# Kernel tuning notes

Measured on AMD Instinct MI355X. Metric: run time of the kernel, lower is better.

## Reference

```python
import jax, jax.numpy as jnp
import numpy as np

N = 50000   # total nodes
E = 600000  # total edges
F = 128     # in_features == hidden_features
H = 128
L = 4       # layers_count
B = 256     # number of graphs in batch
M = 200     # molecule_features
OUT = 12    # out_features
MH = H // 4 # molecular head width


def setup_inputs() -> dict:
    key = jax.random.key(0)
    ks = jax.random.split(key, 16)
    x = jax.random.normal(ks[0], (N, F), dtype=jnp.float32)
    edge_index = jax.random.randint(ks[1], (2, E), 0, N, dtype=jnp.int64)
    # sorted segment ids; guarantee every graph has >=1 node
    batch = jnp.sort(jnp.concatenate([
        jnp.arange(B, dtype=jnp.int64),
        jax.random.randint(ks[2], (N - B,), 0, B, dtype=jnp.int64)]))
    molecule_features = jax.random.normal(ks[3], (B, M), dtype=jnp.float32)
    s = 0.05
    Ws = jax.random.normal(ks[4], (L, H, H), dtype=jnp.float32) * s
    bs = jnp.zeros((L, H), dtype=jnp.float32)
    Wm = jax.random.normal(ks[5], (M, MH), dtype=jnp.float32) * s
    bm = jnp.zeros((MH,), dtype=jnp.float32)
    gamma = jnp.ones((MH,), dtype=jnp.float32)   # BatchNorm1d affine (eval mode, running stats 0/1)
    beta = jnp.zeros((MH,), dtype=jnp.float32)
    W1 = jax.random.normal(ks[6], (2 * H + MH, H), dtype=jnp.float32) * s  # mlp in = 288
    b1 = jnp.zeros((H,), dtype=jnp.float32)
    W2 = jax.random.normal(ks[7], (H, OUT), dtype=jnp.float32) * s
    b2 = jnp.zeros((OUT,), dtype=jnp.float32)
    return dict(x=x, edge_index=edge_index, batch=batch,
                molecule_features=molecule_features, Ws=Ws, bs=bs,
                Wm=Wm, bm=bm, gamma=gamma, beta=beta,
                W1=W1, b1=b1, W2=W2, b2=b2)


def gcn_conv(x, src, dst, W, b):
    # GCNConv: D^{-1/2} (A + I) D^{-1/2} X W + b, degrees include self loops
    ones = jnp.ones((E,), dtype=x.dtype)
    deg = jax.ops.segment_sum(ones, dst, num_segments=N) + 1.0  # self loop
    dis = jax.lax.rsqrt(deg)
    norm = dis[src] * dis[dst]                      # [E]
    xw = x @ W                                      # [N,H]
    msg = xw[src] * norm[:, None]                   # gather + scale
    agg = jax.ops.segment_sum(msg, dst, num_segments=N)
    agg = agg + xw * (dis * dis)[:, None]           # self-loop term
    return agg + b


def reference(x, edge_index, batch, molecule_features, Ws, bs, Wm, bm,
              gamma, beta, W1, b1, W2, b2):
    src, dst = edge_index[0], edge_index[1]
    h = x
    for l in range(L):
        y = jax.nn.relu(gcn_conv(h, src, dst, Ws[l], bs[l]))
        h = y + h  # residual (in == hidden); dropout is identity in eval
    max_pool = jax.ops.segment_max(h, batch, num_segments=B)
    add_pool = jax.ops.segment_sum(h, batch, num_segments=B)
    # molecular head: Linear -> Dropout(eval=identity) -> BatchNorm1d(eval) -> ReLU
    mol = molecule_features @ Wm + bm
    mol = jax.nn.relu(mol * gamma + beta)  # running_mean=0, running_var=1
    z = jnp.concatenate((max_pool, add_pool, mol), axis=1)  # [B, 288]
    z = jax.nn.relu(z @ W1 + b1)
    return z @ W2 + b2  # [B, OUT]
```

## Files before the change

kernel.cpp:

```cpp
#include <hip/hip_runtime.h>
#include <math.h>

static constexpr int NN  = 50000;
static constexpr int NE  = 600000;
static constexpr int HD  = 128;
static constexpr int NL  = 4;
static constexpr int NB  = 256;
static constexpr int NM  = 200;
static constexpr int NO  = 12;
static constexpr int NMH = 32;

#define MAX4(ac, b) { (ac).x = fmaxf((ac).x,(b).x); (ac).y = fmaxf((ac).y,(b).y); (ac).z = fmaxf((ac).z,(b).z); (ac).w = fmaxf((ac).w,(b).w); }
#define ADD4(ac, b) { (ac).x += (b).x; (ac).y += (b).y; (ac).z += (b).z; (ac).w += (b).w; }

typedef short bfx8 __attribute__((ext_vector_type(8)));
typedef float f32x4 __attribute__((ext_vector_type(4)));

__device__ __forceinline__ unsigned short f2bf(float f) {
  unsigned int u = __float_as_uint(f);
  unsigned int r = (u + 0x7fffu + ((u >> 16) & 1u)) >> 16;
  return (unsigned short)r;
}
__device__ __forceinline__ float bflo(unsigned int p) { return __uint_as_float(p << 16); }
__device__ __forceinline__ float bfhi(unsigned int p) { return __uint_as_float(p & 0xffff0000u); }

__global__ void k_hist(const int* __restrict__ dst, int* __restrict__ counts) {
  int e = blockIdx.x * blockDim.x + threadIdx.x;
  if (e < NE) atomicAdd(&counts[dst[e]], 1);
}

__global__ void k_dis(const int* __restrict__ counts, float* __restrict__ dis) {
  int i = blockIdx.x * blockDim.x + threadIdx.x;
  if (i < NN) dis[i] = rsqrtf((float)(counts[i] + 1));
}

__global__ void k_scan1(const int* __restrict__ counts, int* __restrict__ incl, int* __restrict__ bsum) {
  __shared__ int s[256];
  int i = blockIdx.x * 256 + threadIdx.x;
  int v = (i < NN) ? counts[i] : 0;
  s[threadIdx.x] = v;
  __syncthreads();
  for (int off = 1; off < 256; off <<= 1) {
    int t = (threadIdx.x >= off) ? s[threadIdx.x - off] : 0;
    __syncthreads();
    s[threadIdx.x] += t;
    __syncthreads();
  }
  if (i < NN) incl[i] = s[threadIdx.x];
  if (threadIdx.x == 255) bsum[blockIdx.x] = s[255];
}

__global__ void k_scan2(const int* __restrict__ bsum, int* __restrict__ boff, int nblocks) {
  __shared__ int s[256];
  int v = (threadIdx.x < nblocks) ? bsum[threadIdx.x] : 0;
  s[threadIdx.x] = v;
  __syncthreads();
  for (int off = 1; off < 256; off <<= 1) {
    int t = (threadIdx.x >= off) ? s[threadIdx.x - off] : 0;
    __syncthreads();
    s[threadIdx.x] += t;
    __syncthreads();
  }
  boff[threadIdx.x] = s[threadIdx.x] - v;
}

__global__ void k_scan3(const int* __restrict__ counts, int* __restrict__ rowst, const int* __restrict__ boff) {
  int i = blockIdx.x * 256 + threadIdx.x;
  if (i < NN) {
    rowst[i] = rowst[i] - counts[i] + boff[blockIdx.x];
    if (i == NN - 1) rowst[NN] = NE;
  }
}

__global__ void k_fill(const int* __restrict__ src, const int* __restrict__ dst,
                       const int* __restrict__ rowst, int* __restrict__ cur, int* __restrict__ csr) {
  int e = blockIdx.x * blockDim.x + threadIdx.x;
  if (e < NE) {
    int d = dst[e];
    int p = atomicAdd(&cur[d], 1);
    csr[rowst[d] + p] = src[e];
  }
}

__global__ void k_goffs(const int* __restrict__ batch, int* __restrict__ goffs) {
  int i = blockIdx.x * blockDim.x + threadIdx.x;
  if (i >= NN) return;
  int b = batch[i];
  if (i == 0) {
    for (int g = 0; g <= b; ++g) goffs[g] = 0;
  } else {
    int pb = batch[i - 1];
    for (int g = pb + 1; g <= b; ++g) goffs[g] = i;
  }
  if (i == NN - 1) goffs[NB] = NN;
}

__global__ void k_tobf(const float4* __restrict__ in, ushort4* __restrict__ outb, int n4) {
  int i = blockIdx.x * blockDim.x + threadIdx.x;
  if (i < n4) {
    float4 v = in[i];
    outb[i] = make_ushort4(f2bf(v.x), f2bf(v.y), f2bf(v.z), f2bf(v.w));
  }
}

__global__ void k_wT(const float* __restrict__ Ws, unsigned short* __restrict__ wT) {
  int i = blockIdx.x * blockDim.x + threadIdx.x;
  if (i < NL * HD * HD) {
    int l = i >> 14, rem = i & 16383, n = rem >> 7, k = rem & 127;
    wT[i] = f2bf(Ws[l * 16384 + k * 128 + n]);
  }
}

__launch_bounds__(256)
__global__ void k_gemm_mfma(const unsigned short* __restrict__ A,
                            const unsigned short* __restrict__ WT,
                            unsigned short* __restrict__ C) {
  const int wave = threadIdx.x >> 6;
  const int lane = threadIdx.x & 63;
  const int m_base = blockIdx.x * 128 + wave * 32;
  const int lr = lane & 15;
  const int kg = lane >> 4;

  f32x4 acc[2][8];
#pragma unroll
  for (int mi = 0; mi < 2; ++mi)
#pragma unroll
    for (int nj = 0; nj < 8; ++nj) acc[mi][nj] = (f32x4){0.f, 0.f, 0.f, 0.f};

  int ra0 = m_base + lr;       if (ra0 > NN - 1) ra0 = NN - 1;
  int ra1 = m_base + 16 + lr;  if (ra1 > NN - 1) ra1 = NN - 1;

#pragma unroll
  for (int kb = 0; kb < 4; ++kb) {
    const int k0 = kb * 32 + kg * 8;
    bfx8 a0 = *(const bfx8*)&A[(size_t)ra0 * HD + k0];
    bfx8 a1 = *(const bfx8*)&A[(size_t)ra1 * HD + k0];
#pragma unroll
    for (int nj = 0; nj < 8; ++nj) {
      bfx8 b = *(const bfx8*)&WT[(nj * 16 + lr) * HD + k0];
      acc[0][nj] = __builtin_amdgcn_mfma_f32_16x16x32_bf16(a0, b, acc[0][nj], 0, 0, 0);
      acc[1][nj] = __builtin_amdgcn_mfma_f32_16x16x32_bf16(a1, b, acc[1][nj], 0, 0, 0);
    }
  }

  const int col = lane & 15;
  const int rbase = (lane >> 4) * 4;
#pragma unroll
  for (int mi = 0; mi < 2; ++mi) {
#pragma unroll
    for (int r = 0; r < 4; ++r) {
      int row = m_base + mi * 16 + rbase + r;
      if (row < NN) {
#pragma unroll
        for (int nj = 0; nj < 8; ++nj) {
          C[(size_t)row * HD + nj * 16 + col] = f2bf(acc[mi][nj][r]);
        }
      }
    }
  }
}

__global__ void k_agg(const unsigned short* __restrict__ xw, const float* __restrict__ dis,
                      const int* __restrict__ rowst, const int* __restrict__ csr,
                      const float* __restrict__ bias, const float* __restrict__ hin,
                      float* __restrict__ hout, unsigned short* __restrict__ houtb) {
  int g = threadIdx.x >> 5;
  int lane = threadIdx.x & 31;
  int n = blockIdx.x * 8 + g;
  if (n >= NN) return;

  const uint2* xwb = (const uint2*)xw;

  float dn = dis[n];
  float4 acc;
  {
    uint2 p = xwb[(size_t)n * 32 + lane];
    float sl = dn * dn;
    acc.x = bflo(p.x) * sl; acc.y = bfhi(p.x) * sl;
    acc.z = bflo(p.y) * sl; acc.w = bfhi(p.y) * sl;
  }

  int s0 = rowst[n], s1 = rowst[n + 1];
  int idx = s0;
  for (; idx + 2 <= s1; idx += 2) {
    int sA = csr[idx], sB = csr[idx + 1];
    float nA = dis[sA] * dn;
    float nB = dis[sB] * dn;
    uint2 pA = xwb[(size_t)sA * 32 + lane];
    uint2 pB = xwb[(size_t)sB * 32 + lane];
    acc.x += nA * bflo(pA.x); acc.y += nA * bfhi(pA.x);
    acc.z += nA * bflo(pA.y); acc.w += nA * bfhi(pA.y);
    acc.x += nB * bflo(pB.x); acc.y += nB * bfhi(pB.x);
    acc.z += nB * bflo(pB.y); acc.w += nB * bfhi(pB.y);
  }
  if (idx < s1) {
    int sA = csr[idx];
    float nA = dis[sA] * dn;
    uint2 pA = xwb[(size_t)sA * 32 + lane];
    acc.x += nA * bflo(pA.x); acc.y += nA * bfhi(pA.x);
    acc.z += nA * bflo(pA.y); acc.w += nA * bfhi(pA.y);
  }

  float4 b4 = *(const float4*)&bias[lane * 4];
  float4 hv = *(const float4*)&hin[(size_t)n * HD + lane * 4];
  float4 out;
  out.x = fmaxf(acc.x + b4.x, 0.f) + hv.x;
  out.y = fmaxf(acc.y + b4.y, 0.f) + hv.y;
  out.z = fmaxf(acc.z + b4.z, 0.f) + hv.z;
  out.w = fmaxf(acc.w + b4.w, 0.f) + hv.w;
  *(float4*)&hout[(size_t)n * HD + lane * 4] = out;
  *(ushort4*)&houtb[(size_t)n * HD + lane * 4] =
      make_ushort4(f2bf(out.x), f2bf(out.y), f2bf(out.z), f2bf(out.w));
}

__launch_bounds__(1024)
__global__ void k_pool(const float* __restrict__ h, const int* __restrict__ goffs,
                       float* __restrict__ pooled) {
  __shared__ float4 smax[32][32];
  __shared__ float4 ssum[32][32];
  int g = blockIdx.x;
  int slot = threadIdx.x >> 5;
  int lane = threadIdx.x & 31;
  int a = goffs[g], bnd = goffs[g + 1];

  float4 mx = make_float4(-INFINITY, -INFINITY, -INFINITY, -INFINITY);
  float4 sm = make_float4(0.f, 0.f, 0.f, 0.f);
  for (int i = a + slot; i < bnd; i += 32) {
    float4 v = *(const float4*)&h[(size_t)i * HD + lane * 4];
    MAX4(mx, v);
    ADD4(sm, v);
  }
  smax[slot][lane] = mx;
  ssum[slot][lane] = sm;
  __syncthreads();
#pragma unroll
  for (int off = 16; off >= 1; off >>= 1) {
    if (slot < off) {
      float4 m2 = smax[slot + off][lane];
      float4 s2 = ssum[slot + off][lane];
      float4 m1 = smax[slot][lane];
      float4 s1 = ssum[slot][lane];
      MAX4(m1, m2);
      ADD4(s1, s2);
      smax[slot][lane] = m1;
      ssum[slot][lane] = s1;
    }
    __syncthreads();
  }
  if (slot == 0) {
    *(float4*)&pooled[g * 256 + lane * 4]       = smax[0][lane];
    *(float4*)&pooled[g * 256 + 128 + lane * 4] = ssum[0][lane];
  }
}

__global__ void k_head(const float* __restrict__ pooled, const float* __restrict__ mf,
                       const float* __restrict__ Wm, const float* __restrict__ bm,
                       const float* __restrict__ gamma, const float* __restrict__ beta,
                       const float* __restrict__ W1, const float* __restrict__ b1,
                       const float* __restrict__ W2, const float* __restrict__ b2,
                       float* __restrict__ out) {
  __shared__ float z[288];
  __shared__ float z1[128];
  int g = blockIdx.x, t = threadIdx.x;
  z[t] = pooled[g * 256 + t];
  z[128 + t] = pooled[g * 256 + 128 + t];
  if (t < NMH) {
    float acc = bm[t];
    for (int k = 0; k < NM; ++k) acc += mf[g * NM + k] * Wm[k * NMH + t];
    acc = acc * gamma[t] + beta[t];
    z[256 + t] = fmaxf(acc, 0.f);
  }
  __syncthreads();
  float acc = b1[t];
  for (int k = 0; k < 288; ++k) acc += z[k] * W1[k * HD + t];
  z1[t] = fmaxf(acc, 0.f);
  __syncthreads();
  if (t < NO) {
    float a2 = b2[t];
    for (int k = 0; k < HD; ++k) a2 += z1[k] * W2[k * NO + t];
    out[g * NO + t] = a2;
  }
}

extern "C" void kernel_launch(void* const* d_in, const int* in_sizes, int n_in,
                              void* d_out, int out_size, void* d_ws, size_t ws_size,
                              hipStream_t stream) {
  const float* x     = (const float*)d_in[0];
  const int*   eidx  = (const int*)d_in[1];
  const int*   batch = (const int*)d_in[2];
  const float* mf    = (const float*)d_in[3];
  const float* Ws    = (const float*)d_in[4];
  const float* bs    = (const float*)d_in[5];
  const float* Wm    = (const float*)d_in[6];
  const float* bm    = (const float*)d_in[7];
  const float* gamma = (const float*)d_in[8];
  const float* beta  = (const float*)d_in[9];
  const float* W1    = (const float*)d_in[10];
  const float* b1    = (const float*)d_in[11];
  const float* W2    = (const float*)d_in[12];
  const float* b2    = (const float*)d_in[13];
  float* out = (float*)d_out;

  const int* src = eidx;
  const int* dst = eidx + NE;

  char* w = (char*)d_ws;
  size_t off = 0;
  auto alloc = [&](size_t bytes) -> void* {
    void* p = w + off;
    off += (bytes + 255) & ~(size_t)255;
    return p;
  };
  float* dis    = (float*)alloc((size_t)NN * 4);
  float* h      = (float*)alloc((size_t)NN * HD * 4);
  unsigned short* xw  = (unsigned short*)alloc((size_t)NN * HD * 2);
  unsigned short* xbf = (unsigned short*)alloc((size_t)NN * HD * 2);
  unsigned short* hbf = (unsigned short*)alloc((size_t)NN * HD * 2);
  unsigned short* wT  = (unsigned short*)alloc((size_t)NL * HD * HD * 2);
  int* counts   = (int*)alloc((size_t)NN * 4);
  int* cur      = (int*)alloc((size_t)NN * 4);
  int* rowst    = (int*)alloc((size_t)(NN + 1) * 4);
  int* csr      = (int*)alloc((size_t)NE * 4);
  int* bsum     = (int*)alloc(256 * 4);
  int* boff     = (int*)alloc(256 * 4);
  int* goffs    = (int*)alloc((size_t)(NB + 1) * 4);
  float* pooled = (float*)alloc((size_t)NB * 256 * 4);
  (void)ws_size;

  const int SB = (NN + 255) / 256;

  hipMemsetAsync(counts, 0, (size_t)NN * 4, stream);
  hipMemsetAsync(cur, 0, (size_t)NN * 4, stream);

  k_hist<<<(NE + 255) / 256, 256, 0, stream>>>(dst, counts);
  k_dis<<<SB, 256, 0, stream>>>(counts, dis);
  k_scan1<<<SB, 256, 0, stream>>>(counts, rowst, bsum);
  k_scan2<<<1, 256, 0, stream>>>(bsum, boff, SB);
  k_scan3<<<SB, 256, 0, stream>>>(counts, rowst, boff);
  k_fill<<<(NE + 255) / 256, 256, 0, stream>>>(src, dst, rowst, cur, csr);

  k_goffs<<<SB, 256, 0, stream>>>(batch, goffs);
  k_tobf<<<((NN * HD / 4) + 255) / 256, 256, 0, stream>>>((const float4*)x, (ushort4*)xbf, NN * HD / 4);
  k_wT<<<(NL * HD * HD + 255) / 256, 256, 0, stream>>>(Ws, wT);

  for (int l = 0; l < NL; ++l) {
    const unsigned short* gin_bf = (l == 0) ? xbf : hbf;
    const float* resid = (l == 0) ? x : h;
    k_gemm_mfma<<<(NN + 127) / 128, 256, 0, stream>>>(gin_bf, wT + (size_t)l * HD * HD, xw);
    k_agg<<<(NN + 7) / 8, 256, 0, stream>>>(xw, dis, rowst, csr, bs + (size_t)l * HD, resid, h, hbf);
  }

  k_pool<<<NB, 1024, 0, stream>>>(h, goffs, pooled);
  k_head<<<NB, 128, 0, stream>>>(pooled, mf, Wm, bm, gamma, beta, W1, b1, W2, b2, out);
}
```

Baseline: 315.5 us.

## Store residual only in bf16, pack source norm into CSR, unroll aggregation by four

The fp32 hidden-state buffer is removed. The residual is read from, and pooling runs on, the bf16 copy, which halves the per-layer residual read and write traffic. Each CSR entry now carries the source index together with its precomputed inverse-sqrt degree, so the aggregation loop no longer does a dependent gather of dis. The k_dis kernel is folded into the scan, and the edge loop is unrolled by four for more memory-level parallelism. The cost is lower precision in the residual chain and pooled features, plus a CSR array twice as large.

```diff
diff --git a/kernel.cpp b/kernel.cpp
--- a/kernel.cpp
+++ b/kernel.cpp
@@ -29,15 +29,12 @@
   if (e < NE) atomicAdd(&counts[dst[e]], 1);
 }
 
-__global__ void k_dis(const int* __restrict__ counts, float* __restrict__ dis) {
-  int i = blockIdx.x * blockDim.x + threadIdx.x;
-  if (i < NN) dis[i] = rsqrtf((float)(counts[i] + 1));
-}
-
-__global__ void k_scan1(const int* __restrict__ counts, int* __restrict__ incl, int* __restrict__ bsum) {
+__global__ void k_scan1(const int* __restrict__ counts, int* __restrict__ incl,
+                        int* __restrict__ bsum, float* __restrict__ dis) {
   __shared__ int s[256];
   int i = blockIdx.x * 256 + threadIdx.x;
   int v = (i < NN) ? counts[i] : 0;
+  if (i < NN) dis[i] = rsqrtf((float)(v + 1));
   s[threadIdx.x] = v;
   __syncthreads();
   for (int off = 1; off < 256; off <<= 1) {
@@ -73,12 +70,14 @@
 }
 
 __global__ void k_fill(const int* __restrict__ src, const int* __restrict__ dst,
-                       const int* __restrict__ rowst, int* __restrict__ cur, int* __restrict__ csr) {
+                       const int* __restrict__ rowst, const float* __restrict__ dis,
+                       int* __restrict__ cur, uint2* __restrict__ csr) {
   int e = blockIdx.x * blockDim.x + threadIdx.x;
   if (e < NE) {
     int d = dst[e];
+    int s = src[e];
     int p = atomicAdd(&cur[d], 1);
-    csr[rowst[d] + p] = src[e];
+    csr[rowst[d] + p] = make_uint2((unsigned)s, __float_as_uint(dis[s]));
   }
 }
 
@@ -161,9 +160,9 @@
 }
 
 __global__ void k_agg(const unsigned short* __restrict__ xw, const float* __restrict__ dis,
-                      const int* __restrict__ rowst, const int* __restrict__ csr,
-                      const float* __restrict__ bias, const float* __restrict__ hin,
-                      float* __restrict__ hout, unsigned short* __restrict__ houtb) {
+                      const int* __restrict__ rowst, const uint2* __restrict__ csr,
+                      const float* __restrict__ bias, const unsigned short* __restrict__ hinb,
+                      unsigned short* __restrict__ houtb) {
   int g = threadIdx.x >> 5;
   int lane = threadIdx.x & 31;
   int n = blockIdx.x * 8 + g;
@@ -182,39 +181,46 @@
 
   int s0 = rowst[n], s1 = rowst[n + 1];
   int idx = s0;
-  for (; idx + 2 <= s1; idx += 2) {
-    int sA = csr[idx], sB = csr[idx + 1];
-    float nA = dis[sA] * dn;
-    float nB = dis[sB] * dn;
-    uint2 pA = xwb[(size_t)sA * 32 + lane];
-    uint2 pB = xwb[(size_t)sB * 32 + lane];
+  for (; idx + 4 <= s1; idx += 4) {
+    uint2 eA = csr[idx], eB = csr[idx + 1], eC = csr[idx + 2], eD = csr[idx + 3];
+    uint2 pA = xwb[(size_t)eA.x * 32 + lane];
+    uint2 pB = xwb[(size_t)eB.x * 32 + lane];
+    uint2 pC = xwb[(size_t)eC.x * 32 + lane];
+    uint2 pD = xwb[(size_t)eD.x * 32 + lane];
+    float nA = __uint_as_float(eA.y) * dn;
+    float nB = __uint_as_float(eB.y) * dn;
+    float nC = __uint_as_float(eC.y) * dn;
+    float nD = __uint_as_float(eD.y) * dn;
     acc.x += nA * bflo(pA.x); acc.y += nA * bfhi(pA.x);
     acc.z += nA * bflo(pA.y); acc.w += nA * bfhi(pA.y);
     acc.x += nB * bflo(pB.x); acc.y += nB * bfhi(pB.x);
     acc.z += nB * bflo(pB.y); acc.w += nB * bfhi(pB.y);
-  }
-  if (idx < s1) {
-    int sA = csr[idx];
-    float nA = dis[sA] * dn;
-    uint2 pA = xwb[(size_t)sA * 32 + lane];
+    acc.x += nC * bflo(pC.x); acc.y += nC * bfhi(pC.x);
+    acc.z += nC * bflo(pC.y); acc.w += nC * bfhi(pC.y);
+    acc.x += nD * bflo(pD.x); acc.y += nD * bfhi(pD.x);
+    acc.z += nD * bflo(pD.y); acc.w += nD * bfhi(pD.y);
+  }
+  for (; idx < s1; ++idx) {
+    uint2 eA = csr[idx];
+    uint2 pA = xwb[(size_t)eA.x * 32 + lane];
+    float nA = __uint_as_float(eA.y) * dn;
     acc.x += nA * bflo(pA.x); acc.y += nA * bfhi(pA.x);
     acc.z += nA * bflo(pA.y); acc.w += nA * bfhi(pA.y);
   }
 
   float4 b4 = *(const float4*)&bias[lane * 4];
-  float4 hv = *(const float4*)&hin[(size_t)n * HD + lane * 4];
-  float4 out;
-  out.x = fmaxf(acc.x + b4.x, 0.f) + hv.x;
-  out.y = fmaxf(acc.y + b4.y, 0.f) + hv.y;
-  out.z = fmaxf(acc.z + b4.z, 0.f) + hv.z;
-  out.w = fmaxf(acc.w + b4.w, 0.f) + hv.w;
-  *(float4*)&hout[(size_t)n * HD + lane * 4] = out;
+  uint2 hp = ((const uint2*)hinb)[(size_t)n * 32 + lane];
+  float4 outv;
+  outv.x = fmaxf(acc.x + b4.x, 0.f) + bflo(hp.x);
+  outv.y = fmaxf(acc.y + b4.y, 0.f) + bfhi(hp.x);
+  outv.z = fmaxf(acc.z + b4.z, 0.f) + bflo(hp.y);
+  outv.w = fmaxf(acc.w + b4.w, 0.f) + bfhi(hp.y);
   *(ushort4*)&houtb[(size_t)n * HD + lane * 4] =
-      make_ushort4(f2bf(out.x), f2bf(out.y), f2bf(out.z), f2bf(out.w));
+      make_ushort4(f2bf(outv.x), f2bf(outv.y), f2bf(outv.z), f2bf(outv.w));
 }
 
 __launch_bounds__(1024)
-__global__ void k_pool(const float* __restrict__ h, const int* __restrict__ goffs,
+__global__ void k_pool(const unsigned short* __restrict__ hb, const int* __restrict__ goffs,
                        float* __restrict__ pooled) {
   __shared__ float4 smax[32][32];
   __shared__ float4 ssum[32][32];
@@ -222,11 +228,13 @@
   int slot = threadIdx.x >> 5;
   int lane = threadIdx.x & 31;
   int a = goffs[g], bnd = goffs[g + 1];
+  const uint2* hb2 = (const uint2*)hb;
 
   float4 mx = make_float4(-INFINITY, -INFINITY, -INFINITY, -INFINITY);
   float4 sm = make_float4(0.f, 0.f, 0.f, 0.f);
   for (int i = a + slot; i < bnd; i += 32) {
-    float4 v = *(const float4*)&h[(size_t)i * HD + lane * 4];
+    uint2 p = hb2[(size_t)i * 32 + lane];
+    float4 v = make_float4(bflo(p.x), bfhi(p.x), bflo(p.y), bfhi(p.y));
     MAX4(mx, v);
     ADD4(sm, v);
   }
@@ -312,7 +320,6 @@
     return p;
   };
   float* dis    = (float*)alloc((size_t)NN * 4);
-  float* h      = (float*)alloc((size_t)NN * HD * 4);
   unsigned short* xw  = (unsigned short*)alloc((size_t)NN * HD * 2);
   unsigned short* xbf = (unsigned short*)alloc((size_t)NN * HD * 2);
   unsigned short* hbf = (unsigned short*)alloc((size_t)NN * HD * 2);
@@ -320,7 +327,7 @@
   int* counts   = (int*)alloc((size_t)NN * 4);
   int* cur      = (int*)alloc((size_t)NN * 4);
   int* rowst    = (int*)alloc((size_t)(NN + 1) * 4);
-  int* csr      = (int*)alloc((size_t)NE * 4);
+  uint2* csr    = (uint2*)alloc((size_t)NE * 8);
   int* bsum     = (int*)alloc(256 * 4);
   int* boff     = (int*)alloc(256 * 4);
   int* goffs    = (int*)alloc((size_t)(NB + 1) * 4);
@@ -333,11 +340,10 @@
   hipMemsetAsync(cur, 0, (size_t)NN * 4, stream);
 
   k_hist<<<(NE + 255) / 256, 256, 0, stream>>>(dst, counts);
-  k_dis<<<SB, 256, 0, stream>>>(counts, dis);
-  k_scan1<<<SB, 256, 0, stream>>>(counts, rowst, bsum);
+  k_scan1<<<SB, 256, 0, stream>>>(counts, rowst, bsum, dis);
   k_scan2<<<1, 256, 0, stream>>>(bsum, boff, SB);
   k_scan3<<<SB, 256, 0, stream>>>(counts, rowst, boff);
-  k_fill<<<(NE + 255) / 256, 256, 0, stream>>>(src, dst, rowst, cur, csr);
+  k_fill<<<(NE + 255) / 256, 256, 0, stream>>>(src, dst, rowst, dis, cur, csr);
 
   k_goffs<<<SB, 256, 0, stream>>>(batch, goffs);
   k_tobf<<<((NN * HD / 4) + 255) / 256, 256, 0, stream>>>((const float4*)x, (ushort4*)xbf, NN * HD / 4);
@@ -345,11 +351,10 @@
 
   for (int l = 0; l < NL; ++l) {
     const unsigned short* gin_bf = (l == 0) ? xbf : hbf;
-    const float* resid = (l == 0) ? x : h;
     k_gemm_mfma<<<(NN + 127) / 128, 256, 0, stream>>>(gin_bf, wT + (size_t)l * HD * HD, xw);
-    k_agg<<<(NN + 7) / 8, 256, 0, stream>>>(xw, dis, rowst, csr, bs + (size_t)l * HD, resid, h, hbf);
-  }
-
-  k_pool<<<NB, 1024, 0, stream>>>(h, goffs, pooled);
+    k_agg<<<(NN + 7) / 8, 256, 0, stream>>>(xw, dis, rowst, csr, bs + (size_t)l * HD, gin_bf, hbf);
+  }
+
+  k_pool<<<NB, 1024, 0, stream>>>(hbf, goffs, pooled);
   k_head<<<NB, 128, 0, stream>>>(pooled, mf, Wm, bm, gamma, beta, W1, b1, W2, b2, out);
 }
```

Measured after the change: 291.5 us. 7.6% less time.
